# Performance work log

Measured on AMD Instinct MI355X. Metric: run time of the kernel, lower is better.

Reference implementation:

```python
import jax, jax.numpy as jnp
import numpy as np

B, C, L, D, E, K = 64, 23, 26000, 64, 512, 3  # batch, chromosomes, bins/chr, d_model, eos_dim, num_states
V = C * L


def setup_inputs() -> dict:
    key = jax.random.key(0)
    k0, k1, k2, k3 = jax.random.split(key, 4)
    return {
        "eos_emb": jax.random.normal(k0, (B, C, E), jnp.float32),
        "bin_ids": jnp.arange(C * L, dtype=jnp.int32).reshape(C, L),
        "emb_table": jax.random.normal(k1, (V, D), jnp.float32) * 0.02,
        "eos_W": jax.random.normal(k2, (D, E), jnp.float32) / np.float32(np.sqrt(E)),
        "eos_b": jnp.zeros((D,), jnp.float32),
        "fc_W": jax.random.normal(k3, (K, 2 * D), jnp.float32) / np.float32(np.sqrt(2 * D)),
        "fc_b": jnp.zeros((K,), jnp.float32),
    }


def reference(eos_emb, bin_ids, emb_table, eos_W, eos_b, fc_W, fc_b):
    # eos_projection (use_eos_proj=True): [B,C,E] @ [D,E]^T + b -> [B,C,D]
    eos = jnp.einsum('bce,de->bcd', eos_emb, eos_W) + eos_b
    # per-chromosome embedding gather (bin_projection skipped: bin_emb_dim == d_model, use_bin_proj=False)
    bin_emb = emb_table[bin_ids]  # [C,L,D]
    # fc on concat([bin, eos]) == bin @ Wb^T + eos @ We^T + b (avoids materializing [B,C,L,2D])
    Wb, We = fc_W[:, :D], fc_W[:, D:]
    a = jnp.einsum('cld,kd->clk', bin_emb, Wb)          # [C,L,K]
    e = jnp.einsum('bcd,kd->bck', eos, We) + fc_b       # [B,C,K]
    return jax.nn.relu(a[None, :, :, :] + e[:, :, None, :])  # [B,C,L,K]
```

## Files before the change

kernel.cpp:

```cpp
#include <hip/hip_runtime.h>

#define NB 64
#define NC 23
#define NL 26000
#define ND 64
#define NE 512
#define NK 3

__global__ __launch_bounds__(64) void eos_e_kernel(
    const float* __restrict__ eos_emb,
    const float* __restrict__ eos_W,
    const float* __restrict__ eos_b,
    const float* __restrict__ fc_W,
    const float* __restrict__ fc_b,
    float* __restrict__ e_out)
{
    const int bc = blockIdx.x;
    const int d  = threadIdx.x;

    __shared__ float xs[NE];
    float4* xs4 = reinterpret_cast<float4*>(xs);
    const float4* src = reinterpret_cast<const float4*>(eos_emb + (size_t)bc * NE);
    for (int i = d; i < NE / 4; i += 64) xs4[i] = src[i];
    __syncthreads();

    const float4* wrow = reinterpret_cast<const float4*>(eos_W + (size_t)d * NE);
    float acc = 0.f;
    #pragma unroll 8
    for (int i = 0; i < NE / 4; ++i) {
        float4 w = wrow[i];
        float4 x = xs4[i];
        acc += w.x * x.x;
        acc += w.y * x.y;
        acc += w.z * x.z;
        acc += w.w * x.w;
    }
    const float eosd = acc + eos_b[d];

    #pragma unroll
    for (int k = 0; k < NK; ++k) {
        float p = eosd * fc_W[k * (2 * ND) + ND + d];
        #pragma unroll
        for (int off = 32; off > 0; off >>= 1) p += __shfl_xor(p, off, 64);
        if (d == 0) e_out[(size_t)bc * NK + k] = p + fc_b[k];
    }
}

__global__ __launch_bounds__(256) void a_kernel(
    const int*   __restrict__ bin_ids,
    const float* __restrict__ emb_table,
    const float* __restrict__ fc_W,
    float* __restrict__ a_out)
{
    const int c   = blockIdx.y;
    const int tid = threadIdx.x;
    const int l   = blockIdx.x * 256 + tid;

    __shared__ float wb[NK][ND];
    if (tid < NK * ND)
        wb[tid / ND][tid % ND] = fc_W[(tid / ND) * (2 * ND) + (tid % ND)];
    __syncthreads();
    if (l >= NL) return;

    const int row = bin_ids[(size_t)c * NL + l];
    const float4* er = reinterpret_cast<const float4*>(emb_table + (size_t)row * ND);
    const float4* w0 = reinterpret_cast<const float4*>(wb[0]);
    const float4* w1 = reinterpret_cast<const float4*>(wb[1]);
    const float4* w2 = reinterpret_cast<const float4*>(wb[2]);

    float a0 = 0.f, a1 = 0.f, a2 = 0.f;
    #pragma unroll
    for (int i = 0; i < ND / 4; ++i) {
        float4 v  = er[i];
        float4 p0 = w0[i], p1 = w1[i], p2 = w2[i];
        a0 += v.x * p0.x + v.y * p0.y + v.z * p0.z + v.w * p0.w;
        a1 += v.x * p1.x + v.y * p1.y + v.z * p1.z + v.w * p1.w;
        a2 += v.x * p2.x + v.y * p2.y + v.z * p2.z + v.w * p2.w;
    }

    float* dst = a_out + ((size_t)c * NL + l) * NK;
    dst[0] = a0; dst[1] = a1; dst[2] = a2;
}

__global__ __launch_bounds__(256) void store_kernel(
    const float* __restrict__ a_in,
    const float* __restrict__ e_in,
    float* __restrict__ out)
{
    const int c   = blockIdx.y;
    const int tid = threadIdx.x;
    const int l   = blockIdx.x * 256 + tid;

    __shared__ float es[NB * NK];
    if (tid < NB * NK) {
        int b = tid / NK, k = tid % NK;
        es[tid] = e_in[((size_t)b * NC + c) * NK + k];
    }
    __syncthreads();
    if (l >= NL) return;

    const float* ap = a_in + ((size_t)c * NL + l) * NK;
    const float a0 = ap[0], a1 = ap[1], a2 = ap[2];

    size_t obase = ((size_t)c * NL + l) * NK;
    const size_t bstride = (size_t)NC * NL * NK;
    #pragma unroll 8
    for (int b = 0; b < NB; ++b) {
        const float e0 = es[b * NK + 0];
        const float e1 = es[b * NK + 1];
        const float e2 = es[b * NK + 2];
        out[obase + 0] = fmaxf(a0 + e0, 0.f);
        out[obase + 1] = fmaxf(a1 + e1, 0.f);
        out[obase + 2] = fmaxf(a2 + e2, 0.f);
        obase += bstride;
    }
}

__global__ __launch_bounds__(256) void decoder_fused_kernel(
    const int*   __restrict__ bin_ids,
    const float* __restrict__ emb_table,
    const float* __restrict__ fc_W,
    const float* __restrict__ e_in,
    float* __restrict__ out)
{
    const int c   = blockIdx.y;
    const int tid = threadIdx.x;
    const int l   = blockIdx.x * 256 + tid;

    __shared__ float wb[NK][ND];
    __shared__ float es[NB * NK];

    if (tid < NK * ND)
        wb[tid / ND][tid % ND] = fc_W[(tid / ND) * (2 * ND) + (tid % ND)];
    if (tid < NB * NK) {
        int b = tid / NK, k = tid % NK;
        es[tid] = e_in[((size_t)b * NC + c) * NK + k];
    }
    __syncthreads();
    if (l >= NL) return;

    const int row = bin_ids[(size_t)c * NL + l];
    const float4* er = reinterpret_cast<const float4*>(emb_table + (size_t)row * ND);
    const float4* w0 = reinterpret_cast<const float4*>(wb[0]);
    const float4* w1 = reinterpret_cast<const float4*>(wb[1]);
    const float4* w2 = reinterpret_cast<const float4*>(wb[2]);

    float a0 = 0.f, a1 = 0.f, a2 = 0.f;
    #pragma unroll
    for (int i = 0; i < ND / 4; ++i) {
        float4 v  = er[i];
        float4 p0 = w0[i], p1 = w1[i], p2 = w2[i];
        a0 += v.x * p0.x + v.y * p0.y + v.z * p0.z + v.w * p0.w;
        a1 += v.x * p1.x + v.y * p1.y + v.z * p1.z + v.w * p1.w;
        a2 += v.x * p2.x + v.y * p2.y + v.z * p2.z + v.w * p2.w;
    }

    size_t obase = ((size_t)c * NL + l) * NK;
    const size_t bstride = (size_t)NC * NL * NK;
    #pragma unroll 4
    for (int b = 0; b < NB; ++b) {
        const float e0 = es[b * NK + 0];
        const float e1 = es[b * NK + 1];
        const float e2 = es[b * NK + 2];
        out[obase + 0] = fmaxf(a0 + e0, 0.f);
        out[obase + 1] = fmaxf(a1 + e1, 0.f);
        out[obase + 2] = fmaxf(a2 + e2, 0.f);
        obase += bstride;
    }
}

extern "C" void kernel_launch(void* const* d_in, const int* in_sizes, int n_in,
                              void* d_out, int out_size, void* d_ws, size_t ws_size,
                              hipStream_t stream) {
    const float* eos_emb   = (const float*)d_in[0];
    const int*   bin_ids   = (const int*)  d_in[1];
    const float* emb_table = (const float*)d_in[2];
    const float* eos_W     = (const float*)d_in[3];
    const float* eos_b     = (const float*)d_in[4];
    const float* fc_W      = (const float*)d_in[5];
    const float* fc_b      = (const float*)d_in[6];
    float*       out       = (float*)d_out;

    float*  e_ws = (float*)d_ws;
    const size_t a_off_bytes = 32768;
    float*  a_ws = (float*)((char*)d_ws + a_off_bytes);
    const size_t a_bytes = (size_t)NC * NL * NK * sizeof(float);

    eos_e_kernel<<<NB * NC, 64, 0, stream>>>(eos_emb, eos_W, eos_b, fc_W, fc_b, e_ws);

    dim3 grid((NL + 255) / 256, NC);
    if (ws_size >= a_off_bytes + a_bytes) {
        a_kernel<<<grid, 256, 0, stream>>>(bin_ids, emb_table, fc_W, a_ws);
        store_kernel<<<grid, 256, 0, stream>>>(a_ws, e_ws, out);
    } else {
        decoder_fused_kernel<<<grid, 256, 0, stream>>>(bin_ids, emb_table, fc_W, e_ws, out);
    }
}
```

Before: 175.1 us.

## Vectorize broadcast store kernel with float4 rotated e-patterns and nontemporal stores

Replaces the scalar three-float-per-thread store kernel with one that treats each chromosome's [L,K] slab as float4 chunks. Each thread handles three float4 positions and picks the right e-vector from shared memory, where the K=3 bias is pre-rotated into three phase patterns. Loads and stores use nontemporal builtins. The goal is full-width coalesced 16-byte writes for the roughly 460MB output in place of strided 4-byte scalar stores, at the cost of more complex indexing and a reworked grid.

```diff
diff --git a/kernel.cpp b/kernel.cpp
--- a/kernel.cpp
+++ b/kernel.cpp
@@ -6,6 +6,11 @@
 #define ND 64
 #define NE 512
 #define NK 3
+#define NCL (NC * NL)
+#define FP4 (NL * NK / 4)
+#define BSTRIDE4 ((size_t)NC * FP4)
+
+typedef float v4f __attribute__((ext_vector_type(4)));
 
 __global__ __launch_bounds__(64) void eos_e_kernel(
     const float* __restrict__ eos_emb,
@@ -82,37 +87,81 @@
     dst[0] = a0; dst[1] = a1; dst[2] = a2;
 }
 
-__global__ __launch_bounds__(256) void store_kernel(
+__global__ __launch_bounds__(256) void bstream_kernel(
     const float* __restrict__ a_in,
     const float* __restrict__ e_in,
     float* __restrict__ out)
 {
-    const int c   = blockIdx.y;
-    const int tid = threadIdx.x;
-    const int l   = blockIdx.x * 256 + tid;
-
-    __shared__ float es[NB * NK];
-    if (tid < NB * NK) {
-        int b = tid / NK, k = tid % NK;
-        es[tid] = e_in[((size_t)b * NC + c) * NK + k];
-    }
-    __syncthreads();
-    if (l >= NL) return;
-
-    const float* ap = a_in + ((size_t)c * NL + l) * NK;
-    const float a0 = ap[0], a1 = ap[1], a2 = ap[2];
-
-    size_t obase = ((size_t)c * NL + l) * NK;
-    const size_t bstride = (size_t)NC * NL * NK;
-    #pragma unroll 8
+    const int c  = blockIdx.y;
+    const int bx = blockIdx.x;
+    const int t  = threadIdx.x;
+
+    __shared__ v4f e4[3][66];
+    if (t < 3 * NB) {
+        const int p = t >> 6;
+        const int b = t & 63;
+        const float* ep = e_in + ((size_t)b * NC + c) * NK;
+        const float e0 = ep[0], e1 = ep[1], e2 = ep[2];
+        v4f v;
+        if      (p == 0) { v.x = e0; v.y = e1; v.z = e2; v.w = e0; }
+        else if (p == 1) { v.x = e1; v.y = e2; v.z = e0; v.w = e1; }
+        else             { v.x = e2; v.y = e0; v.z = e1; v.w = e2; }
+        e4[p][b] = v;
+    }
+    __syncthreads();
+
+    const int f0 = bx * 768 + t;
+    const int f1 = f0 + 256;
+    const int f2 = f0 + 512;
+    const bool g0 = f0 < FP4, g1 = f1 < FP4, g2 = f2 < FP4;
+
+    const v4f* a4 = reinterpret_cast<const v4f*>(a_in) + (size_t)c * FP4;
+    v4f av0 = (v4f)(0.f), av1 = (v4f)(0.f), av2 = (v4f)(0.f);
+    if (g0) av0 = __builtin_nontemporal_load(&a4[f0]);
+    if (g1) av1 = __builtin_nontemporal_load(&a4[f1]);
+    if (g2) av2 = __builtin_nontemporal_load(&a4[f2]);
+
+    const v4f* ep0 = &e4[f0 % 3][0];
+    const v4f* ep1 = &e4[f1 % 3][0];
+    const v4f* ep2 = &e4[f2 % 3][0];
+
+    v4f* o4 = reinterpret_cast<v4f*>(out);
+    size_t i0 = (size_t)c * FP4 + f0;
+    size_t i1 = (size_t)c * FP4 + f1;
+    size_t i2 = (size_t)c * FP4 + f2;
+
+    #pragma unroll 4
     for (int b = 0; b < NB; ++b) {
-        const float e0 = es[b * NK + 0];
-        const float e1 = es[b * NK + 1];
-        const float e2 = es[b * NK + 2];
-        out[obase + 0] = fmaxf(a0 + e0, 0.f);
-        out[obase + 1] = fmaxf(a1 + e1, 0.f);
-        out[obase + 2] = fmaxf(a2 + e2, 0.f);
-        obase += bstride;
+        if (g0) {
+            const v4f ev = ep0[b];
+            v4f o;
+            o.x = fmaxf(av0.x + ev.x, 0.f);
+            o.y = fmaxf(av0.y + ev.y, 0.f);
+            o.z = fmaxf(av0.z + ev.z, 0.f);
+            o.w = fmaxf(av0.w + ev.w, 0.f);
+            __builtin_nontemporal_store(o, &o4[i0]);
+        }
+        if (g1) {
+            const v4f ev = ep1[b];
+            v4f o;
+            o.x = fmaxf(av1.x + ev.x, 0.f);
+            o.y = fmaxf(av1.y + ev.y, 0.f);
+            o.z = fmaxf(av1.z + ev.z, 0.f);
+            o.w = fmaxf(av1.w + ev.w, 0.f);
+            __builtin_nontemporal_store(o, &o4[i1]);
+        }
+        if (g2) {
+            const v4f ev = ep2[b];
+            v4f o;
+            o.x = fmaxf(av2.x + ev.x, 0.f);
+            o.y = fmaxf(av2.y + ev.y, 0.f);
+            o.z = fmaxf(av2.z + ev.z, 0.f);
+            o.w = fmaxf(av2.w + ev.w, 0.f);
+            __builtin_nontemporal_store(o, &o4[i2]);
+        }
+        i0 += BSTRIDE4;
+        i1 += BSTRIDE4;
+        i2 += BSTRIDE4;
     }
 }
 
@@ -188,11 +237,14 @@
 
     eos_e_kernel<<<NB * NC, 64, 0, stream>>>(eos_emb, eos_W, eos_b, fc_W, fc_b, e_ws);
 
-    dim3 grid((NL + 255) / 256, NC);
     if (ws_size >= a_off_bytes + a_bytes) {
-        a_kernel<<<grid, 256, 0, stream>>>(bin_ids, emb_table, fc_W, a_ws);
-        store_kernel<<<grid, 256, 0, stream>>>(a_ws, e_ws, out);
+        dim3 grid_a((NL + 255) / 256, NC);
+        a_kernel<<<grid_a, 256, 0, stream>>>(bin_ids, emb_table, fc_W, a_ws);
+
+        dim3 grid_b((FP4 + 767) / 768, NC);
+        bstream_kernel<<<grid_b, 256, 0, stream>>>(a_ws, e_ws, out);
     } else {
+        dim3 grid((NL + 255) / 256, NC);
         decoder_fused_kernel<<<grid, 256, 0, stream>>>(bin_ids, emb_table, fc_W, e_ws, out);
     }
 }
```

Result: faster. 162.0 us (-7.5%).
